# Optimization experiments

Measured on AMD Instinct MI355X. Metric: run time of the kernel, lower is better.

The kernel has to match this reference:

```python
import jax, jax.numpy as jnp
import numpy as np

N = 100000        # nodes
E = 1600000       # edges (avg degree 16)
H = 128           # gnn_hidden_size
F_NODE = 4        # node_features (forced to 4 by _validate_and_fix_data)
F_EDGE = 2        # edge_features (forced to 2)
L = 3             # gnn_layers
BN_EPS = 1e-5
NORM_EPS = 1e-12


def _sage_layer(h, src, dst, eattr, Wn, Ws, gamma, beta):
    # message: lin_neighbor(concat(x_j, edge_attr)) where x_j = h[src]
    msg = jnp.concatenate([h[src], eattr], axis=-1) @ Wn          # [E+N, H]
    agg = jax.ops.segment_sum(msg, dst, num_segments=N)           # scatter-sum
    cnt = jax.ops.segment_sum(jnp.ones(dst.shape[0], h.dtype), dst, num_segments=N)
    agg = agg / jnp.maximum(cnt, 1.0)[:, None]                    # mean aggregation
    out = jax.nn.relu(agg + h @ Ws)                               # self-loop linear + ReLU
    # BatchNorm1d (batch statistics, biased var)
    mean = out.mean(axis=0)
    var = out.var(axis=0)
    out = (out - mean) * jax.lax.rsqrt(var + BN_EPS) * gamma + beta
    # dropout = identity (eval); L2 normalize per node
    nrm = jnp.maximum(jnp.linalg.norm(out, axis=-1, keepdims=True), NORM_EPS)
    return out / nrm


def setup_inputs() -> dict:
    key = jax.random.key(0)
    ks = jax.random.split(key, 24)
    s = 0.05
    inp = {
        "x": jax.random.normal(ks[0], (N, F_NODE), jnp.float32),
        "edge_index": jax.random.randint(ks[1], (2, E), 0, N, dtype=jnp.int32),
        "edge_attr": jax.random.uniform(ks[2], (E, F_EDGE), jnp.float32),
        "W_in": jax.random.normal(ks[3], (F_NODE, H), jnp.float32) * s,
        "b_in": jnp.zeros((H,), jnp.float32),
        "W_jump": jax.random.normal(ks[4], (L * H, H), jnp.float32) * s,
        "b_jump": jnp.zeros((H,), jnp.float32),
        "W1": jax.random.normal(ks[5], (H, H // 2), jnp.float32) * s,
        "b1": jnp.zeros((H // 2,), jnp.float32),
        "W2": jax.random.normal(ks[6], (H // 2, 1), jnp.float32) * s,
        "b2": jnp.zeros((1,), jnp.float32),
    }
    for l in range(L):
        inp[f"Wn_{l}"] = jax.random.normal(ks[7 + 4 * l], (H + F_EDGE, H), jnp.float32) * s
        inp[f"Ws_{l}"] = jax.random.normal(ks[8 + 4 * l], (H, H), jnp.float32) * s
        inp[f"gamma_{l}"] = jnp.ones((H,), jnp.float32)
        inp[f"beta_{l}"] = jnp.zeros((H,), jnp.float32)
    return inp


def reference(x, edge_index, edge_attr, W_in, b_in,
              Wn_0, Ws_0, gamma_0, beta_0,
              Wn_1, Ws_1, gamma_1, beta_1,
              Wn_2, Ws_2, gamma_2, beta_2,
              W_jump, b_jump, W1, b1, W2, b2):
    # add self loops (with zero edge_attr), as in _safe_add_self_loops
    loop = jnp.arange(N, dtype=edge_index.dtype)
    src = jnp.concatenate([edge_index[0], loop])
    dst = jnp.concatenate([edge_index[1], loop])
    eattr = jnp.concatenate([edge_attr, jnp.zeros((N, F_EDGE), edge_attr.dtype)], axis=0)

    h = x @ W_in + b_in                                          # input_projection
    layer_params = [(Wn_0, Ws_0, gamma_0, beta_0),
                    (Wn_1, Ws_1, gamma_1, beta_1),
                    (Wn_2, Ws_2, gamma_2, beta_2)]
    layer_outputs = []
    for Wn, Ws, gamma, beta in layer_params:
        h = _sage_layer(h, src, dst, eattr, Wn, Ws, gamma, beta)
        layer_outputs.append(h)
    # jump (skip) connection: concat all layer outputs -> Linear -> ReLU
    h = jax.nn.relu(jnp.concatenate(layer_outputs, axis=-1) @ W_jump + b_jump)
    # neighbor_scorer: Linear -> ReLU -> Linear -> scalar per node
    scores = jax.nn.relu(h @ W1 + b1) @ W2 + b2                  # [N, 1]
    return scores[:, 0]
```

## Files before the change

kernel.cpp:

```cpp
#include <hip/hip_runtime.h>


#define HDIM 128

using f16x8 = __attribute__((ext_vector_type(8))) _Float16;
using f16x4 = __attribute__((ext_vector_type(4))) _Float16;
using f32x4 = __attribute__((ext_vector_type(4))) float;

__device__ inline unsigned pack_f16x2(float a, float b) {
  _Float16 ha = (_Float16)a, hb = (_Float16)b;
  unsigned short ua = __builtin_bit_cast(unsigned short, ha);
  unsigned short ub = __builtin_bit_cast(unsigned short, hb);
  return (unsigned)ua | ((unsigned)ub << 16);
}
__device__ inline float2 unpack_f16x2(unsigned u) {
  _Float16 lo = __builtin_bit_cast(_Float16, (unsigned short)(u & 0xffffu));
  _Float16 hi = __builtin_bit_cast(_Float16, (unsigned short)(u >> 16));
  return make_float2((float)lo, (float)hi);
}

__global__ __launch_bounds__(256) void count_kernel(
    const int* __restrict__ dst, int* __restrict__ cnt, int E) {
  int e = blockIdx.x * 256 + threadIdx.x;
  if (e >= E) return;
  atomicAdd(&cnt[dst[e]], 1);
}

__global__ __launch_bounds__(128) void scan_block_sum(
    const int* __restrict__ cnt, int* __restrict__ bsum, int N) {
  __shared__ int sd[128];
  int t = threadIdx.x;
  int i = blockIdx.x * 128 + t;
  sd[t] = (i < N) ? cnt[i] : 0;
  __syncthreads();
  for (int off = 64; off > 0; off >>= 1) {
    if (t < off) sd[t] += sd[t + off];
    __syncthreads();
  }
  if (t == 0) bsum[blockIdx.x] = sd[0];
}

__global__ __launch_bounds__(256) void scan_partials(
    const int* __restrict__ bsum, int* __restrict__ boff, int nch) {
  __shared__ int sd[256];
  int t = threadIdx.x;
  int base = t * 4;
  int v0 = (base + 0 < nch) ? bsum[base + 0] : 0;
  int v1 = (base + 1 < nch) ? bsum[base + 1] : 0;
  int v2 = (base + 2 < nch) ? bsum[base + 2] : 0;
  int v3 = (base + 3 < nch) ? bsum[base + 3] : 0;
  sd[t] = v0 + v1 + v2 + v3;
  __syncthreads();
  for (int off = 1; off < 256; off <<= 1) {
    int x = sd[t];
    int y = (t >= off) ? sd[t - off] : 0;
    __syncthreads();
    sd[t] = x + y;
    __syncthreads();
  }
  int run = (t == 0) ? 0 : sd[t - 1];
  if (base + 0 < nch) boff[base + 0] = run; run += v0;
  if (base + 1 < nch) boff[base + 1] = run; run += v1;
  if (base + 2 < nch) boff[base + 2] = run; run += v2;
  if (base + 3 < nch) boff[base + 3] = run;
}

__global__ __launch_bounds__(128) void scan_final(
    const int* __restrict__ cnt, const int* __restrict__ boff,
    int* __restrict__ rs, int* __restrict__ rc, int N) {
  __shared__ int sd[128];
  int t = threadIdx.x, b = blockIdx.x;
  int i = b * 128 + t;
  int v = (i < N) ? cnt[i] : 0;
  sd[t] = v;
  __syncthreads();
  for (int off = 1; off < 128; off <<= 1) {
    int x = sd[t];
    int y = (t >= off) ? sd[t - off] : 0;
    __syncthreads();
    sd[t] = x + y;
    __syncthreads();
  }
  int excl = boff[b] + ((t == 0) ? 0 : sd[t - 1]);
  if (i < N) { rs[i] = excl; rc[i] = excl; }
}

__global__ __launch_bounds__(256) void fill_kernel(
    const int* __restrict__ src, const int* __restrict__ dst,
    const float* __restrict__ ea, int* __restrict__ rc,
    uint2* __restrict__ cidx2, int E) {
  int e = blockIdx.x * 256 + threadIdx.x;
  if (e >= E) return;
  int d = dst[e];
  float2 v = *reinterpret_cast<const float2*>(&ea[2 * (size_t)e]);
  int pos = atomicAdd(&rc[d], 1);
  cidx2[pos] = make_uint2((unsigned)src[e], pack_f16x2(v.x, v.y));
}

__global__ __launch_bounds__(256) void aggx_kernel(
    const float* __restrict__ x, const int* __restrict__ rs,
    const int* __restrict__ re, const uint2* __restrict__ cidx2,
    float* __restrict__ aggx, float* __restrict__ eagg, int N) {
  int i = blockIdx.x * 256 + threadIdx.x;
  if (i >= N) return;
  float4 a = *reinterpret_cast<const float4*>(&x[(size_t)i * 4]);
  float4 b = make_float4(0.f, 0.f, 0.f, 0.f);
  float e0 = 0.f, e1 = 0.f, f0 = 0.f, f1 = 0.f;
  int p = rs[i], e = re[i];
  for (; p + 1 < e; p += 2) {
    uint2 c0 = cidx2[p], c1 = cidx2[p + 1];
    float4 v0 = *reinterpret_cast<const float4*>(&x[(size_t)c0.x * 4]);
    float4 v1 = *reinterpret_cast<const float4*>(&x[(size_t)c1.x * 4]);
    float2 u0 = unpack_f16x2(c0.y);
    float2 u1 = unpack_f16x2(c1.y);
    a.x += v0.x; a.y += v0.y; a.z += v0.z; a.w += v0.w;
    b.x += v1.x; b.y += v1.y; b.z += v1.z; b.w += v1.w;
    e0 += u0.x; e1 += u0.y;
    f0 += u1.x; f1 += u1.y;
  }
  if (p < e) {
    uint2 c0 = cidx2[p];
    float4 v0 = *reinterpret_cast<const float4*>(&x[(size_t)c0.x * 4]);
    float2 u0 = unpack_f16x2(c0.y);
    a.x += v0.x; a.y += v0.y; a.z += v0.z; a.w += v0.w;
    e0 += u0.x; e1 += u0.y;
  }
  a.x += b.x; a.y += b.y; a.z += b.z; a.w += b.w;
  *reinterpret_cast<float4*>(&aggx[(size_t)i * 4]) = a;
  eagg[2 * (size_t)i + 0] = e0 + f0;
  eagg[2 * (size_t)i + 1] = e1 + f1;
}

__global__ __launch_bounds__(256) void csr_agg_kernel(
    const _Float16* __restrict__ h, const int* __restrict__ rs,
    const int* __restrict__ re, const uint2* __restrict__ cidx2,
    const int* __restrict__ cnt, _Float16* __restrict__ aggm, int N) {
  int i = blockIdx.x * 8 + (threadIdx.x >> 5);
  if (i >= N) return;
  int lane = threadIdx.x & 31;
  const f16x4* hb = reinterpret_cast<const f16x4*>(h) + lane;
  f16x4 sv = hb[(size_t)i * 32];
  float a0 = (float)sv[0], a1 = (float)sv[1], a2 = (float)sv[2], a3 = (float)sv[3];
  float b0 = 0.f, b1 = 0.f, b2 = 0.f, b3 = 0.f;
  float c0 = 0.f, c1 = 0.f, c2 = 0.f, c3 = 0.f;
  float d0 = 0.f, d1 = 0.f, d2 = 0.f, d3 = 0.f;
  int p = rs[i], e = re[i];
  for (; p + 3 < e; p += 4) {
    uint2 q0 = cidx2[p], q1 = cidx2[p + 1], q2 = cidx2[p + 2], q3 = cidx2[p + 3];
    f16x4 v0 = hb[(size_t)q0.x * 32];
    f16x4 v1 = hb[(size_t)q1.x * 32];
    f16x4 v2 = hb[(size_t)q2.x * 32];
    f16x4 v3 = hb[(size_t)q3.x * 32];
    a0 += (float)v0[0]; a1 += (float)v0[1]; a2 += (float)v0[2]; a3 += (float)v0[3];
    b0 += (float)v1[0]; b1 += (float)v1[1]; b2 += (float)v1[2]; b3 += (float)v1[3];
    c0 += (float)v2[0]; c1 += (float)v2[1]; c2 += (float)v2[2]; c3 += (float)v2[3];
    d0 += (float)v3[0]; d1 += (float)v3[1]; d2 += (float)v3[2]; d3 += (float)v3[3];
  }
  for (; p < e; ++p) {
    uint2 q0 = cidx2[p];
    f16x4 v0 = hb[(size_t)q0.x * 32];
    a0 += (float)v0[0]; a1 += (float)v0[1]; a2 += (float)v0[2]; a3 += (float)v0[3];
  }
  float inv = 1.0f / ((float)cnt[i] + 1.0f);
  f16x4 o;
  o[0] = (_Float16)((a0 + b0 + c0 + d0) * inv);
  o[1] = (_Float16)((a1 + b1 + c1 + d1) * inv);
  o[2] = (_Float16)((a2 + b2 + c2 + d2) * inv);
  o[3] = (_Float16)((a3 + b3 + c3 + d3) * inv);
  (reinterpret_cast<f16x4*>(aggm) + lane)[(size_t)i * 32] = o;
}

__global__ __launch_bounds__(256) void pack_weights_kernel(
    const float* __restrict__ Wn0, const float* __restrict__ Ws0,
    const float* __restrict__ Wn1, const float* __restrict__ Ws1,
    const float* __restrict__ Wn2, const float* __restrict__ Ws2,
    const float* __restrict__ Wj, _Float16* __restrict__ outp) {
  int i = blockIdx.x * 256 + threadIdx.x;
  if (i >= 147456) return;
  int j = i & 7, lane = (i >> 3) & 63;
  float v;
  if (i < 98304) {
    int l = i >> 15;
    int r = i & 32767;
    int nt = (r >> 9) & 7, kt = r >> 12;
    int k = kt * 32 + (lane >> 4) * 8 + j;
    int n = nt * 16 + (lane & 15);
    const float* Wn = (l == 0) ? Wn0 : (l == 1) ? Wn1 : Wn2;
    const float* Ws = (l == 0) ? Ws0 : (l == 1) ? Ws1 : Ws2;
    v = (k < 128) ? Wn[(size_t)k * HDIM + n] : Ws[(size_t)(k - 128) * HDIM + n];
  } else {
    int r = i - 98304;
    int nt = (r >> 9) & 7, kt = r >> 12;
    int k = kt * 32 + (lane >> 4) * 8 + j;
    int n = nt * 16 + (lane & 15);
    v = Wj[(size_t)k * HDIM + n];
  }
  outp[i] = (_Float16)v;
}

template <bool L0>
__global__ __launch_bounds__(256) void sage_mfma_kernel(
    const float* __restrict__ A0f, const float* __restrict__ A1f,
    const _Float16* __restrict__ A0h, const _Float16* __restrict__ A1h,
    const float* __restrict__ Wi, const float* __restrict__ bi,
    const float* __restrict__ eagg, const int* __restrict__ cnt,
    const _Float16* __restrict__ Bp, const float* __restrict__ Wn,
    float* __restrict__ out, float* __restrict__ bnstat, int N) {
  __shared__ _Float16 sA[64 * 256];
  __shared__ float sE[128];
  __shared__ float sBNs[4][128];
  __shared__ float sBNq[4][128];
  const int t = threadIdx.x;
  const int base = blockIdx.x * 64;

  if (t < 64) {
    int grow = base + t;
    float e0 = 0.f, e1 = 0.f;
    if (grow < N) {
      float inv = 1.0f / ((float)cnt[grow] + 1.0f);
      e0 = eagg[2 * (size_t)grow] * inv;
      e1 = eagg[2 * (size_t)grow + 1] * inv;
    }
    sE[2 * t] = e0;
    sE[2 * t + 1] = e1;
  }

#pragma unroll
  for (int it = 0; it < 8; ++it) {
    int c = t + it * 256;
    int row = c >> 5, k8 = c & 31;
    int grow = base + row;
    f16x8 hv = {};
    if (grow < N) {
      if (L0) {
        float inv = 1.0f / ((float)cnt[grow] + 1.0f);
        float scale = (k8 < 16) ? inv : 1.0f;
        const float* rp = (k8 < 16) ? &A0f[(size_t)grow * 4] : &A1f[(size_t)grow * 4];
        float4 r = *reinterpret_cast<const float4*>(rp);
        int col0 = (k8 & 15) * 8;
#pragma unroll
        for (int jj = 0; jj < 8; ++jj) {
          int col = col0 + jj;
          hv[jj] = (_Float16)(bi[col] + scale * (r.x * Wi[col] + r.y * Wi[HDIM + col] +
                                                 r.z * Wi[2 * HDIM + col] + r.w * Wi[3 * HDIM + col]));
        }
      } else {
        hv = (k8 < 16) ? (reinterpret_cast<const f16x8*>(A0h + (size_t)grow * HDIM))[k8]
                       : (reinterpret_cast<const f16x8*>(A1h + (size_t)grow * HDIM))[k8 - 16];
      }
    }
    int byte = (row * 512 + k8 * 16) ^ ((row & 7) << 4);
    *reinterpret_cast<f16x8*>(reinterpret_cast<char*>(sA) + byte) = hv;
  }
  __syncthreads();

  const int lane = t & 63;
  const int w = t >> 6;
  const int col16 = lane & 15;
  const int kgrp = lane >> 4;
  f32x4 acc[8];
#pragma unroll
  for (int nt = 0; nt < 8; ++nt) acc[nt] = (f32x4){0.f, 0.f, 0.f, 0.f};

  const int arow = w * 16 + col16;
  const int aswz = (arow & 7) << 4;
#pragma unroll
  for (int kt = 0; kt < 8; ++kt) {
    int abyte = (arow * 512 + kt * 64 + kgrp * 16) ^ aswz;
    f16x8 a = *reinterpret_cast<const f16x8*>(reinterpret_cast<const char*>(sA) + abyte);
    const f16x8* bp = reinterpret_cast<const f16x8*>(Bp) + (size_t)kt * 512 + lane;
#pragma unroll
    for (int nt = 0; nt < 8; ++nt) {
      f16x8 b = bp[nt * 64];
      acc[nt] = __builtin_amdgcn_mfma_f32_16x16x32_f16(a, b, acc[nt], 0, 0, 0);
    }
  }

#pragma unroll
  for (int nt = 0; nt < 8; ++nt) {
    int col = nt * 16 + col16;
    float we0 = Wn[(size_t)128 * HDIM + col];
    float we1 = Wn[(size_t)129 * HDIM + col];
    float s = 0.f, q = 0.f;
#pragma unroll
    for (int i = 0; i < 4; ++i) {
      int lr = w * 16 + kgrp * 4 + i;
      int row = base + lr;
      if (row < N) {
        float v = acc[nt][i] + sE[2 * lr] * we0 + sE[2 * lr + 1] * we1;
        v = fmaxf(v, 0.f);
        out[(size_t)row * HDIM + col] = v;
        s += v;
        q += v * v;
      }
    }
    s += __shfl_xor(s, 16, 64);
    s += __shfl_xor(s, 32, 64);
    q += __shfl_xor(q, 16, 64);
    q += __shfl_xor(q, 32, 64);
    if (lane < 16) {
      sBNs[w][col] = s;
      sBNq[w][col] = q;
    }
  }
  __syncthreads();
  if (t < 128) {
    float s = sBNs[0][t] + sBNs[1][t] + sBNs[2][t] + sBNs[3][t];
    float q = sBNq[0][t] + sBNq[1][t] + sBNq[2][t] + sBNq[3][t];
    atomicAdd(&bnstat[t], s);
    atomicAdd(&bnstat[HDIM + t], q);
  }
}

__global__ void bn_finalize_kernel(const float* __restrict__ stat,
                                   const float* __restrict__ gamma,
                                   const float* __restrict__ beta,
                                   float* __restrict__ ab, float invN) {
  int j = threadIdx.x;
  float mean = stat[j] * invN;
  float var = stat[128 + j] * invN - mean * mean;
  float inv = 1.0f / sqrtf(var + 1e-5f);
  float A = inv * gamma[j];
  ab[j] = A;
  ab[128 + j] = beta[j] - mean * A;
}

__global__ __launch_bounds__(256) void bn_l2_kernel(const float* __restrict__ outb,
                                                    const float* __restrict__ ab,
                                                    _Float16* __restrict__ h, int N) {
  int i = blockIdx.x * 4 + (threadIdx.x >> 6);
  if (i >= N) return;
  int lane = threadIdx.x & 63;
  float2 v = (reinterpret_cast<const float2*>(outb + (size_t)i * HDIM))[lane];
  float A0 = ab[lane * 2 + 0], A1 = ab[lane * 2 + 1];
  float B0 = ab[128 + lane * 2 + 0], B1 = ab[128 + lane * 2 + 1];
  float y0 = v.x * A0 + B0;
  float y1 = v.y * A1 + B1;
  float s = y0 * y0 + y1 * y1;
#pragma unroll
  for (int m = 32; m > 0; m >>= 1) s += __shfl_xor(s, m, 64);
  float inv = 1.0f / fmaxf(sqrtf(s), 1e-12f);
  (reinterpret_cast<unsigned*>(h + (size_t)i * HDIM))[lane] =
      pack_f16x2(y0 * inv, y1 * inv);
}

__global__ __launch_bounds__(256) void jump_mfma_kernel(
    const _Float16* __restrict__ h1, const _Float16* __restrict__ h2,
    const _Float16* __restrict__ h3, const _Float16* __restrict__ Bp,
    const float* __restrict__ bj, const float* __restrict__ W1p,
    const float* __restrict__ b1p, const float* __restrict__ W2p,
    const float* __restrict__ b2p, float* __restrict__ outp, int N) {
  __shared__ _Float16 sA[64 * 384];
  const int t = threadIdx.x;
  const int base = blockIdx.x * 64;

  const _Float16* hs[3] = {h1, h2, h3};
#pragma unroll
  for (int it = 0; it < 12; ++it) {
    int c = t + it * 256;
    int row = c / 48, k8 = c % 48;
    int grow = base + row;
    f16x8 hv = {};
    if (grow < N)
      hv = (reinterpret_cast<const f16x8*>(hs[k8 >> 4] + (size_t)grow * HDIM))[k8 & 15];
    int byte = (row * 768 + k8 * 16) ^ ((row & 7) << 4);
    *reinterpret_cast<f16x8*>(reinterpret_cast<char*>(sA) + byte) = hv;
  }
  __syncthreads();

  const int lane = t & 63;
  const int w = t >> 6;
  const int col16 = lane & 15;
  const int kgrp = lane >> 4;
  f32x4 acc[8];
#pragma unroll
  for (int nt = 0; nt < 8; ++nt) acc[nt] = (f32x4){0.f, 0.f, 0.f, 0.f};

  const int arow = w * 16 + col16;
  const int aswz = (arow & 7) << 4;
#pragma unroll
  for (int kt = 0; kt < 12; ++kt) {
    int abyte = (arow * 768 + kt * 64 + kgrp * 16) ^ aswz;
    f16x8 a = *reinterpret_cast<const f16x8*>(reinterpret_cast<const char*>(sA) + abyte);
    const f16x8* bp = reinterpret_cast<const f16x8*>(Bp) + (size_t)kt * 512 + lane;
#pragma unroll
    for (int nt = 0; nt < 8; ++nt) {
      f16x8 b = bp[nt * 64];
      acc[nt] = __builtin_amdgcn_mfma_f32_16x16x32_f16(a, b, acc[nt], 0, 0, 0);
    }
  }
  __syncthreads();

  float* sG = reinterpret_cast<float*>(sA);
  float* sS = sG + 64 * 128;
#pragma unroll
  for (int nt = 0; nt < 8; ++nt) {
    int col = nt * 16 + col16;
    float bb = bj[col];
#pragma unroll
    for (int i = 0; i < 4; ++i) {
      int lr = w * 16 + kgrp * 4 + i;
      sG[lr * 128 + col] = fmaxf(acc[nt][i] + bb, 0.f);
    }
  }
  __syncthreads();

  const int m = t & 63, grp = t >> 6;
  float a2[16];
#pragma unroll
  for (int i = 0; i < 16; ++i) a2[i] = b1p[m];
#pragma unroll 4
  for (int k = 0; k < 128; ++k) {
    float wv = W1p[(size_t)k * 64 + m];
#pragma unroll
    for (int i = 0; i < 16; ++i) a2[i] += sG[(grp * 16 + i) * 128 + k] * wv;
  }
#pragma unroll
  for (int i = 0; i < 16; ++i) sS[(grp * 16 + i) * 64 + m] = fmaxf(a2[i], 0.f);
  __syncthreads();

  if (t < 64) {
    int row = base + t;
    if (row < N) {
      float s = b2p[0];
#pragma unroll 8
      for (int mm = 0; mm < 64; ++mm) s += sS[t * 64 + mm] * W2p[mm];
      outp[row] = s;
    }
  }
}

extern "C" void kernel_launch(void* const* d_in, const int* in_sizes, int n_in,
                              void* d_out, int out_size, void* d_ws, size_t ws_size,
                              hipStream_t stream) {
  const float* x      = (const float*)d_in[0];
  const int*   ei     = (const int*)d_in[1];
  const float* eattr  = (const float*)d_in[2];
  const float* W_in   = (const float*)d_in[3];
  const float* b_in   = (const float*)d_in[4];
  const float* W_jump = (const float*)d_in[5];
  const float* b_jump = (const float*)d_in[6];
  const float* W1     = (const float*)d_in[7];
  const float* b1     = (const float*)d_in[8];
  const float* W2     = (const float*)d_in[9];
  const float* b2     = (const float*)d_in[10];
  const float* Wn[3] = {(const float*)d_in[11], (const float*)d_in[15], (const float*)d_in[19]};
  const float* Ws[3] = {(const float*)d_in[12], (const float*)d_in[16], (const float*)d_in[20]};
  const float* gm[3] = {(const float*)d_in[13], (const float*)d_in[17], (const float*)d_in[21]};
  const float* bt[3] = {(const float*)d_in[14], (const float*)d_in[18], (const float*)d_in[22]};

  const int N = in_sizes[0] / 4;
  const int E = in_sizes[2] / 2;
  const int* srcp = ei;
  const int* dstp = ei + (size_t)E;
  const int nch = (N + 127) / 128;
  const size_t nh = (size_t)N * HDIM;

  char* wsb = (char*)d_ws;
  size_t off = 0;
  auto carve = [&](size_t bytes) -> void* {
    void* p = wsb + off;
    off = (off + bytes + 255) & ~(size_t)255;
    return p;
  };
  _Float16* h1   = (_Float16*)carve(nh * 2);
  _Float16* h2   = (_Float16*)carve(nh * 2);
  _Float16* h3   = (_Float16*)carve(nh * 2);
  _Float16* aggm = (_Float16*)carve(nh * 2);
  float*    outb = (float*)carve(nh * 4);
  float*    aggx = (float*)carve((size_t)N * 4 * 4);
  float*    eagg = (float*)carve((size_t)N * 2 * 4);
  int*      cnt  = (int*)carve((size_t)N * 4);
  int*      rowstart = (int*)carve((size_t)N * 4);
  int*      rowcur   = (int*)carve((size_t)N * 4);
  uint2*    cidx2    = (uint2*)carve((size_t)E * 8);
  int*      bsum = (int*)carve(4096);
  int*      boff = (int*)carve(4096);
  float*    bnstat = (float*)carve(1024);
  float*    bnab   = (float*)carve(1024);
  _Float16* wpack  = (_Float16*)carve(147456 * 2);

  hipMemsetAsync(cnt, 0, (size_t)N * sizeof(int), stream);
  count_kernel<<<(E + 255) / 256, 256, 0, stream>>>(dstp, cnt, E);
  pack_weights_kernel<<<(147456 + 255) / 256, 256, 0, stream>>>(
      Wn[0], Ws[0], Wn[1], Ws[1], Wn[2], Ws[2], W_jump, wpack);
  scan_block_sum<<<nch, 128, 0, stream>>>(cnt, bsum, N);
  scan_partials<<<1, 256, 0, stream>>>(bsum, boff, nch);
  scan_final<<<nch, 128, 0, stream>>>(cnt, boff, rowstart, rowcur, N);
  fill_kernel<<<(E + 255) / 256, 256, 0, stream>>>(srcp, dstp, eattr, rowcur, cidx2, E);

  const int gemm_grid = (N + 63) / 64;

  aggx_kernel<<<(N + 255) / 256, 256, 0, stream>>>(x, rowstart, rowcur, cidx2, aggx, eagg, N);
  hipMemsetAsync(bnstat, 0, 256 * sizeof(float), stream);
  sage_mfma_kernel<true><<<gemm_grid, 256, 0, stream>>>(
      aggx, x, nullptr, nullptr, W_in, b_in, eagg, cnt, wpack, Wn[0], outb, bnstat, N);
  bn_finalize_kernel<<<1, 128, 0, stream>>>(bnstat, gm[0], bt[0], bnab, 1.0f / (float)N);
  bn_l2_kernel<<<(N + 3) / 4, 256, 0, stream>>>(outb, bnab, h1, N);

  _Float16* hbuf[3] = {h1, h2, h3};
  for (int l = 1; l < 3; ++l) {
    csr_agg_kernel<<<(N + 7) / 8, 256, 0, stream>>>(hbuf[l - 1], rowstart, rowcur, cidx2,
                                                    cnt, aggm, N);
    hipMemsetAsync(bnstat, 0, 256 * sizeof(float), stream);
    sage_mfma_kernel<false><<<gemm_grid, 256, 0, stream>>>(
        nullptr, nullptr, aggm, hbuf[l - 1], nullptr, nullptr, eagg, cnt,
        wpack + (size_t)l * 32768, Wn[l], outb, bnstat, N);
    bn_finalize_kernel<<<1, 128, 0, stream>>>(bnstat, gm[l], bt[l], bnab, 1.0f / (float)N);
    bn_l2_kernel<<<(N + 3) / 4, 256, 0, stream>>>(outb, bnab, hbuf[l], N);
  }

  jump_mfma_kernel<<<gemm_grid, 256, 0, stream>>>(h1, h2, h3, wpack + 98304, b_jump,
                                                  W1, b1, W2, b2, (float*)d_out, N);
}
```

Before: 656.8 us.

## Fuse CSR aggregation into SAGE GEMM, fp16 intermediates, fold BN finalize

```diff
diff --git a/kernel.cpp b/kernel.cpp
--- a/kernel.cpp
+++ b/kernel.cpp
@@ -4,7 +4,6 @@
 #define HDIM 128
 
 using f16x8 = __attribute__((ext_vector_type(8))) _Float16;
-using f16x4 = __attribute__((ext_vector_type(4))) _Float16;
 using f32x4 = __attribute__((ext_vector_type(4))) float;
 
 __device__ inline unsigned pack_f16x2(float a, float b) {
@@ -20,10 +19,11 @@
 }
 
 __global__ __launch_bounds__(256) void count_kernel(
-    const int* __restrict__ dst, int* __restrict__ cnt, int E) {
+    const int* __restrict__ dst, int* __restrict__ cnt,
+    int* __restrict__ rank, int E) {
   int e = blockIdx.x * 256 + threadIdx.x;
   if (e >= E) return;
-  atomicAdd(&cnt[dst[e]], 1);
+  rank[e] = atomicAdd(&cnt[dst[e]], 1);
 }
 
 __global__ __launch_bounds__(128) void scan_block_sum(
@@ -67,7 +67,7 @@
 
 __global__ __launch_bounds__(128) void scan_final(
     const int* __restrict__ cnt, const int* __restrict__ boff,
-    int* __restrict__ rs, int* __restrict__ rc, int N) {
+    int* __restrict__ rs, int N) {
   __shared__ int sd[128];
   int t = threadIdx.x, b = blockIdx.x;
   int i = b * 128 + t;
@@ -81,32 +81,31 @@
     sd[t] = x + y;
     __syncthreads();
   }
-  int excl = boff[b] + ((t == 0) ? 0 : sd[t - 1]);
-  if (i < N) { rs[i] = excl; rc[i] = excl; }
+  if (i < N) rs[i] = boff[b] + ((t == 0) ? 0 : sd[t - 1]);
 }
 
 __global__ __launch_bounds__(256) void fill_kernel(
     const int* __restrict__ src, const int* __restrict__ dst,
-    const float* __restrict__ ea, int* __restrict__ rc,
-    uint2* __restrict__ cidx2, int E) {
+    const float* __restrict__ ea, const int* __restrict__ rs,
+    const int* __restrict__ rank, uint2* __restrict__ cidx2, int E) {
   int e = blockIdx.x * 256 + threadIdx.x;
   if (e >= E) return;
   int d = dst[e];
   float2 v = *reinterpret_cast<const float2*>(&ea[2 * (size_t)e]);
-  int pos = atomicAdd(&rc[d], 1);
+  int pos = rs[d] + rank[e];
   cidx2[pos] = make_uint2((unsigned)src[e], pack_f16x2(v.x, v.y));
 }
 
 __global__ __launch_bounds__(256) void aggx_kernel(
     const float* __restrict__ x, const int* __restrict__ rs,
-    const int* __restrict__ re, const uint2* __restrict__ cidx2,
+    const int* __restrict__ cnt, const uint2* __restrict__ cidx2,
     float* __restrict__ aggx, float* __restrict__ eagg, int N) {
   int i = blockIdx.x * 256 + threadIdx.x;
   if (i >= N) return;
   float4 a = *reinterpret_cast<const float4*>(&x[(size_t)i * 4]);
   float4 b = make_float4(0.f, 0.f, 0.f, 0.f);
   float e0 = 0.f, e1 = 0.f, f0 = 0.f, f1 = 0.f;
-  int p = rs[i], e = re[i];
+  int p = rs[i], e = p + cnt[i];
   for (; p + 1 < e; p += 2) {
     uint2 c0 = cidx2[p], c1 = cidx2[p + 1];
     float4 v0 = *reinterpret_cast<const float4*>(&x[(size_t)c0.x * 4]);
@@ -129,45 +128,6 @@
   *reinterpret_cast<float4*>(&aggx[(size_t)i * 4]) = a;
   eagg[2 * (size_t)i + 0] = e0 + f0;
   eagg[2 * (size_t)i + 1] = e1 + f1;
-}
-
-__global__ __launch_bounds__(256) void csr_agg_kernel(
-    const _Float16* __restrict__ h, const int* __restrict__ rs,
-    const int* __restrict__ re, const uint2* __restrict__ cidx2,
-    const int* __restrict__ cnt, _Float16* __restrict__ aggm, int N) {
-  int i = blockIdx.x * 8 + (threadIdx.x >> 5);
-  if (i >= N) return;
-  int lane = threadIdx.x & 31;
-  const f16x4* hb = reinterpret_cast<const f16x4*>(h) + lane;
-  f16x4 sv = hb[(size_t)i * 32];
-  float a0 = (float)sv[0], a1 = (float)sv[1], a2 = (float)sv[2], a3 = (float)sv[3];
-  float b0 = 0.f, b1 = 0.f, b2 = 0.f, b3 = 0.f;
-  float c0 = 0.f, c1 = 0.f, c2 = 0.f, c3 = 0.f;
-  float d0 = 0.f, d1 = 0.f, d2 = 0.f, d3 = 0.f;
-  int p = rs[i], e = re[i];
-  for (; p + 3 < e; p += 4) {
-    uint2 q0 = cidx2[p], q1 = cidx2[p + 1], q2 = cidx2[p + 2], q3 = cidx2[p + 3];
-    f16x4 v0 = hb[(size_t)q0.x * 32];
-    f16x4 v1 = hb[(size_t)q1.x * 32];
-    f16x4 v2 = hb[(size_t)q2.x * 32];
-    f16x4 v3 = hb[(size_t)q3.x * 32];
-    a0 += (float)v0[0]; a1 += (float)v0[1]; a2 += (float)v0[2]; a3 += (float)v0[3];
-    b0 += (float)v1[0]; b1 += (float)v1[1]; b2 += (float)v1[2]; b3 += (float)v1[3];
-    c0 += (float)v2[0]; c1 += (float)v2[1]; c2 += (float)v2[2]; c3 += (float)v2[3];
-    d0 += (float)v3[0]; d1 += (float)v3[1]; d2 += (float)v3[2]; d3 += (float)v3[3];
-  }
-  for (; p < e; ++p) {
-    uint2 q0 = cidx2[p];
-    f16x4 v0 = hb[(size_t)q0.x * 32];
-    a0 += (float)v0[0]; a1 += (float)v0[1]; a2 += (float)v0[2]; a3 += (float)v0[3];
-  }
-  float inv = 1.0f / ((float)cnt[i] + 1.0f);
-  f16x4 o;
-  o[0] = (_Float16)((a0 + b0 + c0 + d0) * inv);
-  o[1] = (_Float16)((a1 + b1 + c1 + d1) * inv);
-  o[2] = (_Float16)((a2 + b2 + c2 + d2) * inv);
-  o[3] = (_Float16)((a3 + b3 + c3 + d3) * inv);
-  (reinterpret_cast<f16x4*>(aggm) + lane)[(size_t)i * 32] = o;
 }
 
 __global__ __launch_bounds__(256) void pack_weights_kernel(
@@ -201,11 +161,12 @@
 template <bool L0>
 __global__ __launch_bounds__(256) void sage_mfma_kernel(
     const float* __restrict__ A0f, const float* __restrict__ A1f,
-    const _Float16* __restrict__ A0h, const _Float16* __restrict__ A1h,
+    const _Float16* __restrict__ Hprev, const int* __restrict__ rs,
+    const uint2* __restrict__ cidx2,
     const float* __restrict__ Wi, const float* __restrict__ bi,
     const float* __restrict__ eagg, const int* __restrict__ cnt,
     const _Float16* __restrict__ Bp, const float* __restrict__ Wn,
-    float* __restrict__ out, float* __restrict__ bnstat, int N) {
+    _Float16* __restrict__ outh, float* __restrict__ bnstat, int N) {
   __shared__ _Float16 sA[64 * 256];
   __shared__ float sE[128];
   __shared__ float sBNs[4][128];
@@ -225,14 +186,14 @@
     sE[2 * t + 1] = e1;
   }
 
-#pragma unroll
-  for (int it = 0; it < 8; ++it) {
-    int c = t + it * 256;
-    int row = c >> 5, k8 = c & 31;
-    int grow = base + row;
-    f16x8 hv = {};
-    if (grow < N) {
-      if (L0) {
+  if (L0) {
+#pragma unroll
+    for (int it = 0; it < 8; ++it) {
+      int c = t + it * 256;
+      int row = c >> 5, k8 = c & 31;
+      int grow = base + row;
+      f16x8 hv = {};
+      if (grow < N) {
         float inv = 1.0f / ((float)cnt[grow] + 1.0f);
         float scale = (k8 < 16) ? inv : 1.0f;
         const float* rp = (k8 < 16) ? &A0f[(size_t)grow * 4] : &A1f[(size_t)grow * 4];
@@ -244,13 +205,69 @@
           hv[jj] = (_Float16)(bi[col] + scale * (r.x * Wi[col] + r.y * Wi[HDIM + col] +
                                                  r.z * Wi[2 * HDIM + col] + r.w * Wi[3 * HDIM + col]));
         }
-      } else {
-        hv = (k8 < 16) ? (reinterpret_cast<const f16x8*>(A0h + (size_t)grow * HDIM))[k8]
-                       : (reinterpret_cast<const f16x8*>(A1h + (size_t)grow * HDIM))[k8 - 16];
       }
-    }
-    int byte = (row * 512 + k8 * 16) ^ ((row & 7) << 4);
-    *reinterpret_cast<f16x8*>(reinterpret_cast<char*>(sA) + byte) = hv;
+      int byte = (row * 512 + k8 * 16) ^ ((row & 7) << 4);
+      *reinterpret_cast<f16x8*>(reinterpret_cast<char*>(sA) + byte) = hv;
+    }
+  } else {
+    const int row = t >> 2, q = t & 3;
+    const int grow = base + row;
+    float acc[32];
+#pragma unroll
+    for (int c = 0; c < 32; ++c) acc[c] = 0.f;
+    f16x8 selfv[4] = {};
+    if (grow < N) {
+      const f16x8* selfp = reinterpret_cast<const f16x8*>(Hprev + (size_t)grow * HDIM) + q * 4;
+#pragma unroll
+      for (int j = 0; j < 4; ++j) {
+        selfv[j] = selfp[j];
+#pragma unroll
+        for (int jj = 0; jj < 8; ++jj) acc[j * 8 + jj] = (float)selfv[j][jj];
+      }
+      int p = rs[grow];
+      int e = p + cnt[grow];
+      for (; p + 1 < e; p += 2) {
+        uint2 q0 = cidx2[p], q1 = cidx2[p + 1];
+        const f16x8* n0 = reinterpret_cast<const f16x8*>(Hprev + (size_t)q0.x * HDIM) + q * 4;
+        const f16x8* n1 = reinterpret_cast<const f16x8*>(Hprev + (size_t)q1.x * HDIM) + q * 4;
+        f16x8 c0[4], c1[4];
+#pragma unroll
+        for (int j = 0; j < 4; ++j) c0[j] = n0[j];
+#pragma unroll
+        for (int j = 0; j < 4; ++j) c1[j] = n1[j];
+#pragma unroll
+        for (int j = 0; j < 4; ++j)
+#pragma unroll
+          for (int jj = 0; jj < 8; ++jj)
+            acc[j * 8 + jj] += (float)c0[j][jj] + (float)c1[j][jj];
+      }
+      if (p < e) {
+        uint2 q0 = cidx2[p];
+        const f16x8* n0 = reinterpret_cast<const f16x8*>(Hprev + (size_t)q0.x * HDIM) + q * 4;
+#pragma unroll
+        for (int j = 0; j < 4; ++j) {
+          f16x8 c0 = n0[j];
+#pragma unroll
+          for (int jj = 0; jj < 8; ++jj) acc[j * 8 + jj] += (float)c0[jj];
+        }
+      }
+      float inv = 1.0f / ((float)cnt[grow] + 1.0f);
+#pragma unroll
+      for (int c = 0; c < 32; ++c) acc[c] *= inv;
+    }
+    const int swz = (row & 7) << 4;
+#pragma unroll
+    for (int j = 0; j < 4; ++j) {
+      f16x8 av;
+#pragma unroll
+      for (int jj = 0; jj < 8; ++jj) av[jj] = (_Float16)acc[j * 8 + jj];
+      int k8a = q * 4 + j;
+      *reinterpret_cast<f16x8*>(reinterpret_cast<char*>(sA) +
+                                ((row * 512 + k8a * 16) ^ swz)) = av;
+      int k8h = 16 + q * 4 + j;
+      *reinterpret_cast<f16x8*>(reinterpret_cast<char*>(sA) +
+                                ((row * 512 + k8h * 16) ^ swz)) = selfv[j];
+    }
   }
   __syncthreads();
 
@@ -289,7 +306,7 @@
       if (row < N) {
         float v = acc[nt][i] + sE[2 * lr] * we0 + sE[2 * lr + 1] * we1;
         v = fmaxf(v, 0.f);
-        out[(size_t)row * HDIM + col] = v;
+        outh[(size_t)row * HDIM + col] = (_Float16)v;
         s += v;
         q += v * v;
       }
@@ -312,28 +329,27 @@
   }
 }
 
-__global__ void bn_finalize_kernel(const float* __restrict__ stat,
-                                   const float* __restrict__ gamma,
-                                   const float* __restrict__ beta,
-                                   float* __restrict__ ab, float invN) {
-  int j = threadIdx.x;
-  float mean = stat[j] * invN;
-  float var = stat[128 + j] * invN - mean * mean;
-  float inv = 1.0f / sqrtf(var + 1e-5f);
-  float A = inv * gamma[j];
-  ab[j] = A;
-  ab[128 + j] = beta[j] - mean * A;
-}
-
-__global__ __launch_bounds__(256) void bn_l2_kernel(const float* __restrict__ outb,
-                                                    const float* __restrict__ ab,
-                                                    _Float16* __restrict__ h, int N) {
-  int i = blockIdx.x * 4 + (threadIdx.x >> 6);
+__global__ __launch_bounds__(256) void bn_l2_kernel(
+    const _Float16* __restrict__ outh, const float* __restrict__ stat,
+    const float* __restrict__ gamma, const float* __restrict__ beta,
+    float invN, _Float16* __restrict__ h, int N) {
+  __shared__ float sAB[256];
+  int t = threadIdx.x;
+  if (t < 128) {
+    float mean = stat[t] * invN;
+    float var = stat[128 + t] * invN - mean * mean;
+    float A = gamma[t] / sqrtf(var + 1e-5f);
+    sAB[t] = A;
+    sAB[128 + t] = beta[t] - mean * A;
+  }
+  __syncthreads();
+  int i = blockIdx.x * 4 + (t >> 6);
   if (i >= N) return;
-  int lane = threadIdx.x & 63;
-  float2 v = (reinterpret_cast<const float2*>(outb + (size_t)i * HDIM))[lane];
-  float A0 = ab[lane * 2 + 0], A1 = ab[lane * 2 + 1];
-  float B0 = ab[128 + lane * 2 + 0], B1 = ab[128 + lane * 2 + 1];
+  int lane = t & 63;
+  unsigned u = (reinterpret_cast<const unsigned*>(outh + (size_t)i * HDIM))[lane];
+  float2 v = unpack_f16x2(u);
+  float A0 = sAB[lane * 2 + 0], A1 = sAB[lane * 2 + 1];
+  float B0 = sAB[128 + lane * 2 + 0], B1 = sAB[128 + lane * 2 + 1];
   float y0 = v.x * A0 + B0;
   float y1 = v.y * A1 + B1;
   float s = y0 * y0 + y1 * y1;
@@ -466,48 +482,44 @@
   _Float16* h1   = (_Float16*)carve(nh * 2);
   _Float16* h2   = (_Float16*)carve(nh * 2);
   _Float16* h3   = (_Float16*)carve(nh * 2);
-  _Float16* aggm = (_Float16*)carve(nh * 2);
-  float*    outb = (float*)carve(nh * 4);
+  _Float16* outh = (_Float16*)carve(nh * 2);
   float*    aggx = (float*)carve((size_t)N * 4 * 4);
   float*    eagg = (float*)carve((size_t)N * 2 * 4);
   int*      cnt  = (int*)carve((size_t)N * 4);
   int*      rowstart = (int*)carve((size_t)N * 4);
-  int*      rowcur   = (int*)carve((size_t)N * 4);
+  int*      rank     = (int*)carve((size_t)E * 4);
   uint2*    cidx2    = (uint2*)carve((size_t)E * 8);
   int*      bsum = (int*)carve(4096);
   int*      boff = (int*)carve(4096);
   float*    bnstat = (float*)carve(1024);
-  float*    bnab   = (float*)carve(1024);
   _Float16* wpack  = (_Float16*)carve(147456 * 2);
 
   hipMemsetAsync(cnt, 0, (size_t)N * sizeof(int), stream);
-  count_kernel<<<(E + 255) / 256, 256, 0, stream>>>(dstp, cnt, E);
+  count_kernel<<<(E + 255) / 256, 256, 0, stream>>>(dstp, cnt, rank, E);
   pack_weights_kernel<<<(147456 + 255) / 256, 256, 0, stream>>>(
       Wn[0], Ws[0], Wn[1], Ws[1], Wn[2], Ws[2], W_jump, wpack);
   scan_block_sum<<<nch, 128, 0, stream>>>(cnt, bsum, N);
   scan_partials<<<1, 256, 0, stream>>>(bsum, boff, nch);
-  scan_final<<<nch, 128, 0, stream>>>(cnt, boff, rowstart, rowcur, N);
-  fill_kernel<<<(E + 255) / 256, 256, 0, stream>>>(srcp, dstp, eattr, rowcur, cidx2, E);
+  scan_final<<<nch, 128, 0, stream>>>(cnt, boff, rowstart, N);
+  fill_kernel<<<(E + 255) / 256, 256, 0, stream>>>(srcp, dstp, eattr, rowstart, rank, cidx2, E);
 
   const int gemm_grid = (N + 63) / 64;
-
-  aggx_kernel<<<(N + 255) / 256, 256, 0, stream>>>(x, rowstart, rowcur, cidx2, aggx, eagg, N);
+  const float invN = 1.0f / (float)N;
+
+  aggx_kernel<<<(N + 255) / 256, 256, 0, stream>>>(x, rowstart, cnt, cidx2, aggx, eagg, N);
   hipMemsetAsync(bnstat, 0, 256 * sizeof(float), stream);
   sage_mfma_kernel<true><<<gemm_grid, 256, 0, stream>>>(
-      aggx, x, nullptr, nullptr, W_in, b_in, eagg, cnt, wpack, Wn[0], outb, bnstat, N);
-  bn_finalize_kernel<<<1, 128, 0, stream>>>(bnstat, gm[0], bt[0], bnab, 1.0f / (float)N);
-  bn_l2_kernel<<<(N + 3) / 4, 256, 0, stream>>>(outb, bnab, h1, N);
+      aggx, x, nullptr, rowstart, cidx2, W_in, b_in, eagg, cnt, wpack, Wn[0],
+      outh, bnstat, N);
+  bn_l2_kernel<<<(N + 3) / 4, 256, 0, stream>>>(outh, bnstat, gm[0], bt[0], invN, h1, N);
 
   _Float16* hbuf[3] = {h1, h2, h3};
   for (int l = 1; l < 3; ++l) {
-    csr_agg_kernel<<<(N + 7) / 8, 256, 0, stream>>>(hbuf[l - 1], rowstart, rowcur, cidx2,
-                                                    cnt, aggm, N);
     hipMemsetAsync(bnstat, 0, 256 * sizeof(float), stream);
     sage_mfma_kernel<false><<<gemm_grid, 256, 0, stream>>>(
-        nullptr, nullptr, aggm, hbuf[l - 1], nullptr, nullptr, eagg, cnt,
-        wpack + (size_t)l * 32768, Wn[l], outb, bnstat, N);
-    bn_finalize_kernel<<<1, 128, 0, stream>>>(bnstat, gm[l], bt[l], bnab, 1.0f / (float)N);
-    bn_l2_kernel<<<(N + 3) / 4, 256, 0, stream>>>(outb, bnab, hbuf[l], N);
+        nullptr, nullptr, hbuf[l - 1], rowstart, cidx2, nullptr, nullptr, eagg, cnt,
+        wpack + (size_t)l * 32768, Wn[l], outh, bnstat, N);
+    bn_l2_kernel<<<(N + 3) / 4, 256, 0, stream>>>(outh, bnstat, gm[l], bt[l], invN, hbuf[l], N);
   }
 
   jump_mfma_kernel<<<gemm_grid, 256, 0, stream>>>(h1, h2, h3, wpack + 98304, b_jump,
```

Result: faster. 590.7 us (-10.1%).
